# Kernel tuning notes

Hardware: AMD Instinct MI355X
Metric: run time of the kernel (lower is better)

The kernel has to match this reference:

```python
import jax, jax.numpy as jnp
import numpy as np

B, C, H, W_IMG = 4, 4, 512, 512
OUT_CH = 256
POS_NUM = 512
NEG_NUM = 512
M_MARGIN = 0.5
TAU = 0.1
EPS = 1e-8


def setup_inputs() -> dict:
    key = jax.random.key(0)
    k1, k2, k3, k4, k5, k6 = jax.random.split(key, 6)
    d1_fegc = jax.random.normal(k1, (B, C, H, W_IMG), dtype=jnp.float32)
    p_fegc = jax.random.uniform(k2, (B, 1, H, W_IMG), dtype=jnp.float32)
    p_pre = jax.random.uniform(k3, (B, 3, H, W_IMG), dtype=jnp.float32)
    gt = (jax.random.uniform(k4, (B, 1, H, W_IMG)) < 0.5).astype(jnp.float32)
    # parameters of the nn.Linear(in_channel, out_channel)
    W = jax.random.normal(k5, (OUT_CH, C), dtype=jnp.float32) / np.sqrt(C)
    b_fc = jax.random.normal(k6, (OUT_CH,), dtype=jnp.float32) * 0.01
    return {"d1_fegc": d1_fegc, "p_fegc": p_fegc, "p_pre": p_pre, "gt": gt, "W": W, "b_fc": b_fc}


def _sample_idx(mask_flat, key, n):
    # randomized fixed-size sampling of n indices where mask is True
    # (replaces torch.nonzero + randperm with a jit-friendly top-k over random scores)
    score = jnp.where(mask_flat, jax.random.uniform(key, mask_flat.shape), -jnp.inf)
    _, idx = jax.lax.top_k(score, n)
    return idx


def reference(d1_fegc, p_fegc, p_pre, gt, W, b_fc):
    b, c, h, w = d1_fegc.shape
    P = POS_NUM * b
    N = NEG_NUM * b
    # p_overlap channel 3: fegc foreground AND pre argmax-class 0
    fegc_fg = p_fegc[:, 0] >= 0.5                       # [b,h,w]
    pre_cls0 = jnp.argmax(p_pre, axis=1) == 0           # [b,h,w]
    pre_region = fegc_fg & pre_cls0                     # [b,h,w]
    gt_fg = gt[:, 0] > 0.5                              # [b,h,w]
    pos_mask = (pre_region & gt_fg).reshape(-1)         # [b*h*w]
    neg_mask = (pre_region & ~gt_fg).reshape(-1)        # [b*h*w]
    # per-pixel feature vectors from d1_fegc
    feats = d1_fegc.transpose(0, 2, 3, 1).reshape(-1, c)  # [b*h*w, c]
    skey = jax.random.key(42)
    kp, kn = jax.random.split(skey)
    pos_idx = _sample_idx(pos_mask, kp, P)
    neg_idx = _sample_idx(neg_mask, kn, N)
    pts = jnp.concatenate([feats[pos_idx], feats[neg_idx]], axis=0)  # [P+N, c]
    proj = pts @ W.T + b_fc                                           # [P+N, out]
    # F.cosine_similarity with eps=1e-8 norm clamping
    norm = jnp.maximum(jnp.linalg.norm(proj, axis=-1, keepdims=True), EPS)
    normed = proj / norm
    cos_sim = normed @ normed.T                                       # [P+N, P+N]
    T = P + N
    label = jnp.ones((T, T), dtype=cos_sim.dtype)
    label = label.at[:P, P:].set(0.0).at[P:, :P].set(0.0)
    s = cos_sim / TAU
    lam = (1.0 - label) * jnp.square(s) + label * jnp.square(jnp.maximum(M_MARGIN - s, 0.0))
    lam = lam * (1.0 - jnp.eye(T, dtype=lam.dtype))                   # mask self pairs
    denom = jnp.sum(lam != 0).astype(lam.dtype)
    return jnp.sum(lam) / denom
```

## Files before the change

kernel.cpp:

```cpp
#include <hip/hip_runtime.h>
#include <stdint.h>

#define HW       262144u
#define NPIX     1048576u
#define NSEL     2048u
#define NSEG     1024u
#define SEGCAP   16u
#define DENSECAP 3584u

#define OFF_SEG     0u
#define OFF_IDX     262144u
#define OFF_VA      278528u
#define OFF_WA      360448u
#define OFF_PSUM    442368u
#define OFF_PNNZ    446464u

#define TF_ROUND(r) { x0 += x1; x1 = (x1 << (r)) | (x1 >> (32 - (r))); x1 ^= x0; }
__host__ __device__ inline void threefry2x32_(uint32_t k0, uint32_t k1,
                                              uint32_t& x0, uint32_t& x1) {
  uint32_t k2 = k0 ^ k1 ^ 0x1BD11BDAu;
  x0 += k0; x1 += k1;
  TF_ROUND(13) TF_ROUND(15) TF_ROUND(26) TF_ROUND(6)
  x0 += k1; x1 += k2 + 1u;
  TF_ROUND(17) TF_ROUND(29) TF_ROUND(16) TF_ROUND(24)
  x0 += k2; x1 += k0 + 2u;
  TF_ROUND(13) TF_ROUND(15) TF_ROUND(26) TF_ROUND(6)
  x0 += k0; x1 += k1 + 3u;
  TF_ROUND(17) TF_ROUND(29) TF_ROUND(16) TF_ROUND(24)
  x0 += k1; x1 += k2 + 4u;
  TF_ROUND(13) TF_ROUND(15) TF_ROUND(26) TF_ROUND(6)
  x0 += k2; x1 += k0 + 5u;
}

__global__ __launch_bounds__(256) void k_front(
    const float* __restrict__ pfegc, const float* __restrict__ ppre,
    const float* __restrict__ gt,
    uint32_t kp0, uint32_t kp1, uint32_t kn0, uint32_t kn1,
    uint64_t* __restrict__ seg) {
  __shared__ uint32_t cnt2[2];
  int t = threadIdx.x;
  uint32_t b = blockIdx.x;
  if (t < 2) cnt2[t] = 0;
  if (t < 2 * (int)SEGCAP) {
    uint32_t list = (uint32_t)t / SEGCAP, slot = (uint32_t)t % SEGCAP;
    seg[((size_t)list * NSEG + b) * SEGCAP + slot] = 0ull;
  }
  __syncthreads();
  uint32_t base = b * 1024u + (uint32_t)t * 4u;
  float4 pf = *(const float4*)(pfegc + base);
  float pfa[4] = { pf.x, pf.y, pf.z, pf.w };
  bool any = (pf.x >= 0.5f) || (pf.y >= 0.5f) || (pf.z >= 0.5f) || (pf.w >= 0.5f);
  if (any) {
    uint32_t hw = base & (HW - 1u);
    uint32_t bb = base >> 18;
    const float* pp = ppre + (size_t)bb * 3u * HW + hw;
    float4 p0 = *(const float4*)pp;
    float4 p1 = *(const float4*)(pp + HW);
    float4 p2 = *(const float4*)(pp + 2u * HW);
    float4 g4 = *(const float4*)(gt + base);
    float p0a[4] = { p0.x, p0.y, p0.z, p0.w };
    float p1a[4] = { p1.x, p1.y, p1.z, p1.w };
    float p2a[4] = { p2.x, p2.y, p2.z, p2.w };
    float ga[4]  = { g4.x, g4.y, g4.z, g4.w };
    #pragma unroll
    for (int j = 0; j < 4; ++j) {
      if (pfa[j] >= 0.5f && p0a[j] >= p1a[j] && p0a[j] >= p2a[j]) {
        uint32_t i = base + (uint32_t)j;
        bool gfg = ga[j] > 0.5f;
        uint32_t x0 = 0u, x1 = i;
        threefry2x32_(gfg ? kp0 : kn0, gfg ? kp1 : kn1, x0, x1);
        uint32_t r23 = (x0 ^ x1) >> 9;
        if ((r23 >> 18) == 0x1Fu) {
          uint32_t list = gfg ? 0u : 1u;
          uint32_t r = atomicAdd(&cnt2[list], 1u);
          if (r < SEGCAP)
            seg[((size_t)list * NSEG + b) * SEGCAP + r] =
                (1ull << 43) | ((uint64_t)r23 << 20) | (uint64_t)(0xFFFFFu ^ i);
        }
      }
    }
  }
}

__global__ __launch_bounds__(256) void k_sel(
    const uint64_t* __restrict__ seg, uint32_t* __restrict__ idxbuf) {
  __shared__ uint64_t dense[DENSECAP];
  __shared__ uint32_t hist[2048];
  __shared__ uint32_t part[256];
  __shared__ uint32_t skk, rank, ntot;
  __shared__ int gsel;
  __shared__ uint64_t spref;
  int t = threadIdx.x;
  int list = blockIdx.x;
  uint32_t lane = (uint32_t)t & 63u;
  if (t == 0) { spref = 0ull; skk = NSEL; rank = 0; }
  const uint4* sp4 = (const uint4*)(seg + (size_t)list * NSEG * SEGCAP);
  uint32_t c = 0;
  #pragma unroll
  for (int it = 0; it < 32; ++it) {
    uint4 v = sp4[(uint32_t)it * 256u + (uint32_t)t];
    c += ((v.y >> 11) & 1u) + ((v.w >> 11) & 1u);
  }
  part[t] = c;
  __syncthreads();
  for (int off = 1; off < 256; off <<= 1) {
    uint32_t x = part[t];
    uint32_t add = (t >= off) ? part[t - off] : 0u;
    __syncthreads();
    part[t] = x + add;
    __syncthreads();
  }
  uint32_t wbase = part[t] - c;
  if (t == 255) ntot = part[255];
  #pragma unroll
  for (int it = 0; it < 32; ++it) {
    uint4 v = sp4[(uint32_t)it * 256u + (uint32_t)t];
    uint64_t k0 = ((uint64_t)v.y << 32) | v.x;
    uint64_t k1 = ((uint64_t)v.w << 32) | v.z;
    if (k0 >> 43) { if (wbase < DENSECAP) dense[wbase] = k0; ++wbase; }
    if (k1 >> 43) { if (wbase < DENSECAP) dense[wbase] = k1; ++wbase; }
  }
  __syncthreads();
  uint32_t n = ntot; if (n > DENSECAP) n = DENSECAP;
  for (int r = 0; r < 4; ++r) {
    #pragma unroll
    for (int e = 0; e < 8; ++e) hist[t * 8 + e] = 0;
    __syncthreads();
    int csp = 44 - 11 * r;
    int cs = csp - 11;
    uint64_t pref = spref;
    for (uint32_t j = t; j < n; j += 256) {
      uint64_t key = dense[j];
      if ((key >> csp) == pref)
        atomicAdd(&hist[(uint32_t)(key >> cs) & 0x7FFu], 1u);
    }
    __syncthreads();
    uint32_t ss = 0;
    #pragma unroll
    for (int e = 0; e < 8; ++e) ss += hist[t * 8 + e];
    part[t] = ss;
    __syncthreads();
    for (int off = 1; off < 256; off <<= 1) {
      uint32_t x = part[t];
      uint32_t y = (t + off < 256) ? part[t + off] : 0u;
      __syncthreads();
      part[t] = x + y;
      __syncthreads();
    }
    uint32_t k = skk;
    if (part[t] >= k && (t == 255 || part[t + 1] < k)) gsel = t;
    __syncthreads();
    if (t == 0) {
      int g = gsel;
      uint32_t cum = (g < 255) ? part[g + 1] : 0u;
      int d = g * 8;
      for (int e = g * 8 + 7; e >= g * 8; --e) {
        uint32_t he = hist[e];
        if (cum + he >= k) { d = e; break; }
        cum += he;
      }
      skk = k - cum;
      spref = (pref << 11) | (uint64_t)(uint32_t)d;
    }
    __syncthreads();
  }
  uint64_t thr = spref;
  uint32_t niter = (n + 255u) >> 8;
  for (uint32_t it2 = 0; it2 < niter; ++it2) {
    uint32_t j = it2 * 256u + (uint32_t)t;
    uint64_t key = 0ull;
    bool v = false;
    if (j < n) { key = dense[j]; v = key >= thr; }
    unsigned long long m = __ballot(v);
    uint32_t bs = 0;
    if (lane == 0) bs = atomicAdd(&rank, (uint32_t)__popcll(m));
    bs = (uint32_t)__shfl((int)bs, 0, 64);
    if (v) {
      uint32_t s = bs + (uint32_t)__popcll(m & ((1ull << lane) - 1ull));
      if (s < NSEL)
        idxbuf[(uint32_t)list * NSEL + s] = 0xFFFFFu ^ (uint32_t)(key & 0xFFFFFu);
    }
  }
}

__global__ __launch_bounds__(256) void k_proj(
    const uint32_t* __restrict__ idxbuf, const float* __restrict__ Wm,
    const float* __restrict__ bfc, const float* __restrict__ d1,
    float* __restrict__ va, float* __restrict__ wa) {
  __shared__ float sG[25];
  __shared__ float sGw[4][25];
  int t = threadIdx.x;
  {
    float4 wr = *(const float4*)(Wm + t * 4);
    float av[5] = { wr.x, wr.y, wr.z, wr.w, bfc[t] };
    int lane = t & 63, wvi = t >> 6;
    #pragma unroll
    for (int p = 0; p < 5; ++p)
      #pragma unroll
      for (int q = p; q < 5; ++q) {
        float g = av[p] * av[q];
        #pragma unroll
        for (int off = 32; off > 0; off >>= 1)
          g += __shfl_xor(g, off, 64);
        if (lane == 0) sGw[wvi][p * 5 + q] = g;
      }
  }
  __syncthreads();
  if (t < 25) {
    int p = t / 5, q = t % 5;
    int pp = p < q ? p : q, qq = p < q ? q : p;
    sG[t] = sGw[0][pp * 5 + qq] + sGw[1][pp * 5 + qq]
          + sGw[2][pp * 5 + qq] + sGw[3][pp * 5 + qq];
  }
  __syncthreads();
  uint32_t tg = blockIdx.x * 256u + (uint32_t)t;
  uint32_t idx = idxbuf[tg] & (NPIX - 1u);
  uint32_t hw = idx & (HW - 1u);
  uint32_t bb = idx >> 18;
  const float* f = d1 + ((size_t)bb << 20) + hw;
  float y[5] = { f[0], f[HW], f[2u * HW], f[3u * HW], 1.0f };
  float z[5]; float n2 = 0.f;
  #pragma unroll
  for (int p = 0; p < 5; ++p) {
    float acc = 0.f;
    #pragma unroll
    for (int q = 0; q < 5; ++q) acc += sG[p * 5 + q] * y[q];
    z[p] = acc; n2 += acc * y[p];
  }
  n2 = fmaxf(n2, 0.f);
  float inv = 1.0f / fmaxf(sqrtf(n2), 1e-8f);
  uint32_t s5 = tg * 5u;
  #pragma unroll
  for (int p = 0; p < 5; ++p) {
    va[s5 + p] = y[p] * inv;
    wa[s5 + p] = z[p] * inv;
  }
}

__global__ __launch_bounds__(256) void k_pair(
    const float* __restrict__ va, const float* __restrict__ wa,
    float* __restrict__ psum, uint32_t* __restrict__ pnnz) {
  __shared__ float sv[128 * 5], sw[128 * 5];
  __shared__ float rs[256];
  __shared__ uint32_t rn[256];
  int i0 = blockIdx.x * 128, j0 = blockIdx.y * 128;
  int t = threadIdx.x;
  for (int u = t; u < 640; u += 256) { sv[u] = va[i0 * 5 + u]; sw[u] = wa[j0 * 5 + u]; }
  __syncthreads();
  int ty = t >> 4, tx = t & 15;
  float rv[8][5], rw[8][5];
  #pragma unroll
  for (int a = 0; a < 8; ++a)
    #pragma unroll
    for (int p = 0; p < 5; ++p) {
      rv[a][p] = sv[(ty * 8 + a) * 5 + p];
      rw[a][p] = sw[(tx * 8 + a) * 5 + p];
    }
  float lsum = 0.f; uint32_t lnz = 0;
  #pragma unroll
  for (int a = 0; a < 8; ++a) {
    int gi = i0 + ty * 8 + a;
    #pragma unroll
    for (int q = 0; q < 8; ++q) {
      int gj = j0 + tx * 8 + q;
      float c = rv[a][0]*rw[q][0] + rv[a][1]*rw[q][1] + rv[a][2]*rw[q][2]
              + rv[a][3]*rw[q][3] + rv[a][4]*rw[q][4];
      float s = c * 10.0f;
      if (gi != gj) {
        if (((gi ^ gj) & 2048) == 0) {
          float m = fmaxf(0.5f - s, 0.f);
          lsum += m * m;
          lnz += (m > 0.f) ? 1u : 0u;
        } else {
          lsum += s * s;
          lnz += (s != 0.f) ? 1u : 0u;
        }
      }
    }
  }
  rs[t] = lsum; rn[t] = lnz;
  __syncthreads();
  for (int off = 128; off > 0; off >>= 1) {
    if (t < off) { rs[t] += rs[t + off]; rn[t] += rn[t + off]; }
    __syncthreads();
  }
  if (t == 0) {
    int bid = blockIdx.y * gridDim.x + blockIdx.x;
    psum[bid] = rs[0];
    pnnz[bid] = rn[0];
  }
}

__global__ __launch_bounds__(256) void k_final(const float* __restrict__ psum,
                                               const uint32_t* __restrict__ pnnz,
                                               float* __restrict__ out) {
  __shared__ float rs[256];
  __shared__ uint32_t rn[256];
  int t = threadIdx.x;
  float s = 0.f; uint32_t nz = 0;
  for (int j = t; j < 1024; j += 256) { s += psum[j]; nz += pnnz[j]; }
  rs[t] = s; rn[t] = nz;
  __syncthreads();
  for (int off = 128; off > 0; off >>= 1) {
    if (t < off) { rs[t] += rs[t + off]; rn[t] += rn[t + off]; }
    __syncthreads();
  }
  if (t == 0) out[0] = rs[0] / (float)rn[0];
}

extern "C" void kernel_launch(void* const* d_in, const int* in_sizes, int n_in,
                              void* d_out, int out_size, void* d_ws, size_t ws_size,
                              hipStream_t stream) {
  (void)in_sizes; (void)n_in; (void)out_size; (void)ws_size;
  const float* d1    = (const float*)d_in[0];
  const float* pfegc = (const float*)d_in[1];
  const float* ppre  = (const float*)d_in[2];
  const float* gt    = (const float*)d_in[3];
  const float* W     = (const float*)d_in[4];
  const float* bfc   = (const float*)d_in[5];
  float* out = (float*)d_out;

  uint8_t* base = (uint8_t*)d_ws;
  uint64_t* seg    = (uint64_t*)(base + OFF_SEG);
  uint32_t* idxbuf = (uint32_t*)(base + OFF_IDX);
  float*    va     = (float*)(base + OFF_VA);
  float*    wa     = (float*)(base + OFF_WA);
  float*    psum   = (float*)(base + OFF_PSUM);
  uint32_t* pnnz   = (uint32_t*)(base + OFF_PNNZ);

  uint32_t kp0 = 0u, kp1 = 0u; threefry2x32_(0u, 42u, kp0, kp1);
  uint32_t kn0 = 0u, kn1 = 1u; threefry2x32_(0u, 42u, kn0, kn1);

  k_front<<<NSEG, 256, 0, stream>>>(pfegc, ppre, gt, kp0, kp1, kn0, kn1, seg);
  k_sel<<<2, 256, 0, stream>>>(seg, idxbuf);
  k_proj<<<16, 256, 0, stream>>>(idxbuf, W, bfc, d1, va, wa);
  k_pair<<<dim3(32, 32), 256, 0, stream>>>(va, wa, psum, pnnz);
  k_final<<<1, 256, 0, stream>>>(psum, pnnz, out);
}
```

Before: 125.2 us.

## Fuse all five stages into one cooperative kernel with grid-wide syncs

Replaces the five separate kernel launches with a single cooperative kernel of 512 blocks that runs the front, select, projection, pairwise and final stages, separated by grid.sync. Each block handles two front tiles and two pair tiles, and shared memory is overlaid through a union. The aim is to remove per-launch overhead and the gaps between dependent kernels. In exchange, the serial select and projection stages idle most blocks behind grid barriers, grid.sync itself has a cost, and the larger union shared allocation may limit occupancy. A fallback to the original launches is kept in case the cooperative launch fails.

```diff
diff --git a/kernel.cpp b/kernel.cpp
--- a/kernel.cpp
+++ b/kernel.cpp
@@ -1,5 +1,8 @@
 #include <hip/hip_runtime.h>
+#include <hip/hip_cooperative_groups.h>
 #include <stdint.h>
+
+namespace cg = cooperative_groups;
 
 #define HW       262144u
 #define NPIX     1048576u
@@ -7,6 +10,7 @@
 #define NSEG     1024u
 #define SEGCAP   16u
 #define DENSECAP 3584u
+#define CGRID    512u
 
 #define OFF_SEG     0u
 #define OFF_IDX     262144u
@@ -32,21 +36,44 @@
   x0 += k2; x1 += k0 + 5u;
 }
 
-__global__ __launch_bounds__(256) void k_front(
+struct SelS {
+  uint64_t dense[DENSECAP];
+  uint64_t spref;
+  uint32_t hist[2048];
+  uint32_t part[256];
+  uint32_t skk, rank, ntot;
+  int gsel;
+};
+struct ProjS {
+  float sG[25];
+  float sGw[4][25];
+};
+struct PairS {
+  float sv[640], sw[640];
+  float rs[256];
+  uint32_t rn[256];
+};
+union SMemU {
+  uint32_t cnt2[2];
+  SelS sel;
+  ProjS proj;
+  PairS pair;
+};
+
+
+__device__ inline void front_body(uint32_t tile, int t, SMemU& sm,
     const float* __restrict__ pfegc, const float* __restrict__ ppre,
     const float* __restrict__ gt,
     uint32_t kp0, uint32_t kp1, uint32_t kn0, uint32_t kn1,
     uint64_t* __restrict__ seg) {
-  __shared__ uint32_t cnt2[2];
-  int t = threadIdx.x;
-  uint32_t b = blockIdx.x;
-  if (t < 2) cnt2[t] = 0;
+  __syncthreads();
+  if (t < 2) sm.cnt2[t] = 0;
   if (t < 2 * (int)SEGCAP) {
     uint32_t list = (uint32_t)t / SEGCAP, slot = (uint32_t)t % SEGCAP;
-    seg[((size_t)list * NSEG + b) * SEGCAP + slot] = 0ull;
-  }
-  __syncthreads();
-  uint32_t base = b * 1024u + (uint32_t)t * 4u;
+    seg[((size_t)list * NSEG + tile) * SEGCAP + slot] = 0ull;
+  }
+  __syncthreads();
+  uint32_t base = tile * 1024u + (uint32_t)t * 4u;
   float4 pf = *(const float4*)(pfegc + base);
   float pfa[4] = { pf.x, pf.y, pf.z, pf.w };
   bool any = (pf.x >= 0.5f) || (pf.y >= 0.5f) || (pf.z >= 0.5f) || (pf.w >= 0.5f);
@@ -72,9 +99,9 @@
         uint32_t r23 = (x0 ^ x1) >> 9;
         if ((r23 >> 18) == 0x1Fu) {
           uint32_t list = gfg ? 0u : 1u;
-          uint32_t r = atomicAdd(&cnt2[list], 1u);
+          uint32_t r = atomicAdd(&sm.cnt2[list], 1u);
           if (r < SEGCAP)
-            seg[((size_t)list * NSEG + b) * SEGCAP + r] =
+            seg[((size_t)list * NSEG + tile) * SEGCAP + r] =
                 (1ull << 43) | ((uint64_t)r23 << 20) | (uint64_t)(0xFFFFFu ^ i);
         }
       }
@@ -82,98 +109,90 @@
   }
 }
 
-__global__ __launch_bounds__(256) void k_sel(
+__device__ inline void sel_body(int list, int t, SMemU& sm,
     const uint64_t* __restrict__ seg, uint32_t* __restrict__ idxbuf) {
-  __shared__ uint64_t dense[DENSECAP];
-  __shared__ uint32_t hist[2048];
-  __shared__ uint32_t part[256];
-  __shared__ uint32_t skk, rank, ntot;
-  __shared__ int gsel;
-  __shared__ uint64_t spref;
-  int t = threadIdx.x;
-  int list = blockIdx.x;
   uint32_t lane = (uint32_t)t & 63u;
-  if (t == 0) { spref = 0ull; skk = NSEL; rank = 0; }
+  if (t == 0) { sm.sel.spref = 0ull; sm.sel.skk = NSEL; sm.sel.rank = 0; }
   const uint4* sp4 = (const uint4*)(seg + (size_t)list * NSEG * SEGCAP);
   uint32_t c = 0;
-  #pragma unroll
+  #pragma unroll 8
   for (int it = 0; it < 32; ++it) {
     uint4 v = sp4[(uint32_t)it * 256u + (uint32_t)t];
     c += ((v.y >> 11) & 1u) + ((v.w >> 11) & 1u);
   }
-  part[t] = c;
+  sm.sel.part[t] = c;
   __syncthreads();
   for (int off = 1; off < 256; off <<= 1) {
-    uint32_t x = part[t];
-    uint32_t add = (t >= off) ? part[t - off] : 0u;
-    __syncthreads();
-    part[t] = x + add;
-    __syncthreads();
-  }
-  uint32_t wbase = part[t] - c;
-  if (t == 255) ntot = part[255];
-  #pragma unroll
+    uint32_t x = sm.sel.part[t];
+    uint32_t add = (t >= off) ? sm.sel.part[t - off] : 0u;
+    __syncthreads();
+    sm.sel.part[t] = x + add;
+    __syncthreads();
+  }
+  uint32_t wbase = sm.sel.part[t] - c;
+  if (t == 255) sm.sel.ntot = sm.sel.part[255];
+  #pragma unroll 8
   for (int it = 0; it < 32; ++it) {
     uint4 v = sp4[(uint32_t)it * 256u + (uint32_t)t];
     uint64_t k0 = ((uint64_t)v.y << 32) | v.x;
     uint64_t k1 = ((uint64_t)v.w << 32) | v.z;
-    if (k0 >> 43) { if (wbase < DENSECAP) dense[wbase] = k0; ++wbase; }
-    if (k1 >> 43) { if (wbase < DENSECAP) dense[wbase] = k1; ++wbase; }
-  }
-  __syncthreads();
-  uint32_t n = ntot; if (n > DENSECAP) n = DENSECAP;
+    if (k0 >> 43) { if (wbase < DENSECAP) sm.sel.dense[wbase] = k0; ++wbase; }
+    if (k1 >> 43) { if (wbase < DENSECAP) sm.sel.dense[wbase] = k1; ++wbase; }
+  }
+  __syncthreads();
+  uint32_t n = sm.sel.ntot; if (n > DENSECAP) n = DENSECAP;
   for (int r = 0; r < 4; ++r) {
     #pragma unroll
-    for (int e = 0; e < 8; ++e) hist[t * 8 + e] = 0;
+    for (int e = 0; e < 8; ++e) sm.sel.hist[t * 8 + e] = 0;
     __syncthreads();
     int csp = 44 - 11 * r;
     int cs = csp - 11;
-    uint64_t pref = spref;
+    uint64_t pref = sm.sel.spref;
     for (uint32_t j = t; j < n; j += 256) {
-      uint64_t key = dense[j];
+      uint64_t key = sm.sel.dense[j];
       if ((key >> csp) == pref)
-        atomicAdd(&hist[(uint32_t)(key >> cs) & 0x7FFu], 1u);
+        atomicAdd(&sm.sel.hist[(uint32_t)(key >> cs) & 0x7FFu], 1u);
     }
     __syncthreads();
     uint32_t ss = 0;
     #pragma unroll
-    for (int e = 0; e < 8; ++e) ss += hist[t * 8 + e];
-    part[t] = ss;
+    for (int e = 0; e < 8; ++e) ss += sm.sel.hist[t * 8 + e];
+    sm.sel.part[t] = ss;
     __syncthreads();
     for (int off = 1; off < 256; off <<= 1) {
-      uint32_t x = part[t];
-      uint32_t y = (t + off < 256) ? part[t + off] : 0u;
+      uint32_t x = sm.sel.part[t];
+      uint32_t y = (t + off < 256) ? sm.sel.part[t + off] : 0u;
       __syncthreads();
-      part[t] = x + y;
+      sm.sel.part[t] = x + y;
       __syncthreads();
     }
-    uint32_t k = skk;
-    if (part[t] >= k && (t == 255 || part[t + 1] < k)) gsel = t;
+    uint32_t k = sm.sel.skk;
+    if (sm.sel.part[t] >= k && (t == 255 || sm.sel.part[t + 1] < k)) sm.sel.gsel = t;
     __syncthreads();
     if (t == 0) {
-      int g = gsel;
-      uint32_t cum = (g < 255) ? part[g + 1] : 0u;
+      int g = sm.sel.gsel;
+      uint32_t cum = (g < 255) ? sm.sel.part[g + 1] : 0u;
       int d = g * 8;
       for (int e = g * 8 + 7; e >= g * 8; --e) {
-        uint32_t he = hist[e];
+        uint32_t he = sm.sel.hist[e];
         if (cum + he >= k) { d = e; break; }
         cum += he;
       }
-      skk = k - cum;
-      spref = (pref << 11) | (uint64_t)(uint32_t)d;
-    }
-    __syncthreads();
-  }
-  uint64_t thr = spref;
+      sm.sel.skk = k - cum;
+      sm.sel.spref = (pref << 11) | (uint64_t)(uint32_t)d;
+    }
+    __syncthreads();
+  }
+  uint64_t thr = sm.sel.spref;
   uint32_t niter = (n + 255u) >> 8;
   for (uint32_t it2 = 0; it2 < niter; ++it2) {
     uint32_t j = it2 * 256u + (uint32_t)t;
     uint64_t key = 0ull;
     bool v = false;
-    if (j < n) { key = dense[j]; v = key >= thr; }
+    if (j < n) { key = sm.sel.dense[j]; v = key >= thr; }
     unsigned long long m = __ballot(v);
     uint32_t bs = 0;
-    if (lane == 0) bs = atomicAdd(&rank, (uint32_t)__popcll(m));
+    if (lane == 0) bs = atomicAdd(&sm.sel.rank, (uint32_t)__popcll(m));
     bs = (uint32_t)__shfl((int)bs, 0, 64);
     if (v) {
       uint32_t s = bs + (uint32_t)__popcll(m & ((1ull << lane) - 1ull));
@@ -183,13 +202,10 @@
   }
 }
 
-__global__ __launch_bounds__(256) void k_proj(
+__device__ inline void proj_body(uint32_t pb, int t, SMemU& sm,
     const uint32_t* __restrict__ idxbuf, const float* __restrict__ Wm,
     const float* __restrict__ bfc, const float* __restrict__ d1,
     float* __restrict__ va, float* __restrict__ wa) {
-  __shared__ float sG[25];
-  __shared__ float sGw[4][25];
-  int t = threadIdx.x;
   {
     float4 wr = *(const float4*)(Wm + t * 4);
     float av[5] = { wr.x, wr.y, wr.z, wr.w, bfc[t] };
@@ -202,18 +218,18 @@
         #pragma unroll
         for (int off = 32; off > 0; off >>= 1)
           g += __shfl_xor(g, off, 64);
-        if (lane == 0) sGw[wvi][p * 5 + q] = g;
+        if (lane == 0) sm.proj.sGw[wvi][p * 5 + q] = g;
       }
   }
   __syncthreads();
   if (t < 25) {
     int p = t / 5, q = t % 5;
     int pp = p < q ? p : q, qq = p < q ? q : p;
-    sG[t] = sGw[0][pp * 5 + qq] + sGw[1][pp * 5 + qq]
-          + sGw[2][pp * 5 + qq] + sGw[3][pp * 5 + qq];
-  }
-  __syncthreads();
-  uint32_t tg = blockIdx.x * 256u + (uint32_t)t;
+    sm.proj.sG[t] = sm.proj.sGw[0][pp * 5 + qq] + sm.proj.sGw[1][pp * 5 + qq]
+                  + sm.proj.sGw[2][pp * 5 + qq] + sm.proj.sGw[3][pp * 5 + qq];
+  }
+  __syncthreads();
+  uint32_t tg = pb * 256u + (uint32_t)t;
   uint32_t idx = idxbuf[tg] & (NPIX - 1u);
   uint32_t hw = idx & (HW - 1u);
   uint32_t bb = idx >> 18;
@@ -224,7 +240,7 @@
   for (int p = 0; p < 5; ++p) {
     float acc = 0.f;
     #pragma unroll
-    for (int q = 0; q < 5; ++q) acc += sG[p * 5 + q] * y[q];
+    for (int q = 0; q < 5; ++q) acc += sm.proj.sG[p * 5 + q] * y[q];
     z[p] = acc; n2 += acc * y[p];
   }
   n2 = fmaxf(n2, 0.f);
@@ -237,15 +253,15 @@
   }
 }
 
-__global__ __launch_bounds__(256) void k_pair(
+__device__ inline void pair_body(uint32_t bid, int t, SMemU& sm,
     const float* __restrict__ va, const float* __restrict__ wa,
     float* __restrict__ psum, uint32_t* __restrict__ pnnz) {
-  __shared__ float sv[128 * 5], sw[128 * 5];
-  __shared__ float rs[256];
-  __shared__ uint32_t rn[256];
-  int i0 = blockIdx.x * 128, j0 = blockIdx.y * 128;
-  int t = threadIdx.x;
-  for (int u = t; u < 640; u += 256) { sv[u] = va[i0 * 5 + u]; sw[u] = wa[j0 * 5 + u]; }
+  int i0 = (int)(bid & 31u) * 128;
+  int j0 = (int)(bid >> 5) * 128;
+  for (int u = t; u < 640; u += 256) {
+    sm.pair.sv[u] = va[i0 * 5 + u];
+    sm.pair.sw[u] = wa[j0 * 5 + u];
+  }
   __syncthreads();
   int ty = t >> 4, tx = t & 15;
   float rv[8][5], rw[8][5];
@@ -253,8 +269,8 @@
   for (int a = 0; a < 8; ++a)
     #pragma unroll
     for (int p = 0; p < 5; ++p) {
-      rv[a][p] = sv[(ty * 8 + a) * 5 + p];
-      rw[a][p] = sw[(tx * 8 + a) * 5 + p];
+      rv[a][p] = sm.pair.sv[(ty * 8 + a) * 5 + p];
+      rw[a][p] = sm.pair.sw[(tx * 8 + a) * 5 + p];
     }
   float lsum = 0.f; uint32_t lnz = 0;
   #pragma unroll
@@ -278,34 +294,92 @@
       }
     }
   }
-  rs[t] = lsum; rn[t] = lnz;
+  sm.pair.rs[t] = lsum; sm.pair.rn[t] = lnz;
   __syncthreads();
   for (int off = 128; off > 0; off >>= 1) {
-    if (t < off) { rs[t] += rs[t + off]; rn[t] += rn[t + off]; }
+    if (t < off) { sm.pair.rs[t] += sm.pair.rs[t + off]; sm.pair.rn[t] += sm.pair.rn[t + off]; }
     __syncthreads();
   }
   if (t == 0) {
-    int bid = blockIdx.y * gridDim.x + blockIdx.x;
-    psum[bid] = rs[0];
-    pnnz[bid] = rn[0];
-  }
-}
-
-__global__ __launch_bounds__(256) void k_final(const float* __restrict__ psum,
-                                               const uint32_t* __restrict__ pnnz,
-                                               float* __restrict__ out) {
-  __shared__ float rs[256];
-  __shared__ uint32_t rn[256];
-  int t = threadIdx.x;
+    psum[bid] = sm.pair.rs[0];
+    pnnz[bid] = sm.pair.rn[0];
+  }
+  __syncthreads();
+}
+
+__device__ inline void final_body(int t, SMemU& sm,
+    const float* __restrict__ psum, const uint32_t* __restrict__ pnnz,
+    float* __restrict__ out) {
   float s = 0.f; uint32_t nz = 0;
   for (int j = t; j < 1024; j += 256) { s += psum[j]; nz += pnnz[j]; }
-  rs[t] = s; rn[t] = nz;
+  sm.pair.rs[t] = s; sm.pair.rn[t] = nz;
   __syncthreads();
   for (int off = 128; off > 0; off >>= 1) {
-    if (t < off) { rs[t] += rs[t + off]; rn[t] += rn[t + off]; }
-    __syncthreads();
-  }
-  if (t == 0) out[0] = rs[0] / (float)rn[0];
+    if (t < off) { sm.pair.rs[t] += sm.pair.rs[t + off]; sm.pair.rn[t] += sm.pair.rn[t + off]; }
+    __syncthreads();
+  }
+  if (t == 0) out[0] = sm.pair.rs[0] / (float)sm.pair.rn[0];
+}
+
+__global__ __launch_bounds__(256, 2) void k_fused(
+    const float* __restrict__ pfegc, const float* __restrict__ ppre,
+    const float* __restrict__ gt,
+    uint32_t kp0, uint32_t kp1, uint32_t kn0, uint32_t kn1,
+    const float* __restrict__ Wm, const float* __restrict__ bfc,
+    const float* __restrict__ d1,
+    uint64_t* __restrict__ seg, uint32_t* __restrict__ idxbuf,
+    float* __restrict__ va, float* __restrict__ wa,
+    float* __restrict__ psum, uint32_t* __restrict__ pnnz,
+    float* __restrict__ out) {
+  cg::grid_group grid = cg::this_grid();
+  __shared__ SMemU sm;
+  int t = threadIdx.x;
+  uint32_t b = blockIdx.x;
+
+  front_body(2u * b,      t, sm, pfegc, ppre, gt, kp0, kp1, kn0, kn1, seg);
+  front_body(2u * b + 1u, t, sm, pfegc, ppre, gt, kp0, kp1, kn0, kn1, seg);
+  grid.sync();
+  if (b < 2) sel_body((int)b, t, sm, seg, idxbuf);
+  grid.sync();
+  if (b < 16) proj_body(b, t, sm, idxbuf, Wm, bfc, d1, va, wa);
+  grid.sync();
+  pair_body(b,        t, sm, va, wa, psum, pnnz);
+  pair_body(b + 512u, t, sm, va, wa, psum, pnnz);
+  grid.sync();
+  if (b == 0) final_body(t, sm, psum, pnnz, out);
+}
+
+__global__ __launch_bounds__(256) void k_front(
+    const float* __restrict__ pfegc, const float* __restrict__ ppre,
+    const float* __restrict__ gt,
+    uint32_t kp0, uint32_t kp1, uint32_t kn0, uint32_t kn1,
+    uint64_t* __restrict__ seg) {
+  __shared__ SMemU sm;
+  front_body(blockIdx.x, threadIdx.x, sm, pfegc, ppre, gt, kp0, kp1, kn0, kn1, seg);
+}
+__global__ __launch_bounds__(256) void k_sel(
+    const uint64_t* __restrict__ seg, uint32_t* __restrict__ idxbuf) {
+  __shared__ SMemU sm;
+  sel_body(blockIdx.x, threadIdx.x, sm, seg, idxbuf);
+}
+__global__ __launch_bounds__(256) void k_proj(
+    const uint32_t* __restrict__ idxbuf, const float* __restrict__ Wm,
+    const float* __restrict__ bfc, const float* __restrict__ d1,
+    float* __restrict__ va, float* __restrict__ wa) {
+  __shared__ SMemU sm;
+  proj_body(blockIdx.x, threadIdx.x, sm, idxbuf, Wm, bfc, d1, va, wa);
+}
+__global__ __launch_bounds__(256) void k_pair(
+    const float* __restrict__ va, const float* __restrict__ wa,
+    float* __restrict__ psum, uint32_t* __restrict__ pnnz) {
+  __shared__ SMemU sm;
+  pair_body(blockIdx.x, threadIdx.x, sm, va, wa, psum, pnnz);
+}
+__global__ __launch_bounds__(256) void k_final(
+    const float* __restrict__ psum, const uint32_t* __restrict__ pnnz,
+    float* __restrict__ out) {
+  __shared__ SMemU sm;
+  final_body(threadIdx.x, sm, psum, pnnz, out);
 }
 
 extern "C" void kernel_launch(void* const* d_in, const int* in_sizes, int n_in,
@@ -331,9 +405,21 @@
   uint32_t kp0 = 0u, kp1 = 0u; threefry2x32_(0u, 42u, kp0, kp1);
   uint32_t kn0 = 0u, kn1 = 1u; threefry2x32_(0u, 42u, kn0, kn1);
 
-  k_front<<<NSEG, 256, 0, stream>>>(pfegc, ppre, gt, kp0, kp1, kn0, kn1, seg);
-  k_sel<<<2, 256, 0, stream>>>(seg, idxbuf);
-  k_proj<<<16, 256, 0, stream>>>(idxbuf, W, bfc, d1, va, wa);
-  k_pair<<<dim3(32, 32), 256, 0, stream>>>(va, wa, psum, pnnz);
-  k_final<<<1, 256, 0, stream>>>(psum, pnnz, out);
-}
+  void* args[] = {
+    (void*)&pfegc, (void*)&ppre, (void*)&gt,
+    (void*)&kp0, (void*)&kp1, (void*)&kn0, (void*)&kn1,
+    (void*)&W, (void*)&bfc, (void*)&d1,
+    (void*)&seg, (void*)&idxbuf, (void*)&va, (void*)&wa,
+    (void*)&psum, (void*)&pnnz, (void*)&out
+  };
+  hipError_t e = hipLaunchCooperativeKernel((const void*)k_fused,
+                                            dim3(CGRID), dim3(256),
+                                            args, 0, stream);
+  if (e != hipSuccess) {
+    k_front<<<NSEG, 256, 0, stream>>>(pfegc, ppre, gt, kp0, kp1, kn0, kn1, seg);
+    k_sel<<<2, 256, 0, stream>>>(seg, idxbuf);
+    k_proj<<<16, 256, 0, stream>>>(idxbuf, W, bfc, d1, va, wa);
+    k_pair<<<1024, 256, 0, stream>>>(va, wa, psum, pnnz);
+    k_final<<<1, 256, 0, stream>>>(psum, pnnz, out);
+  }
+}
```

Result: slower. 326.8 us (+161.0%).
